# Performance work log

Measured on AMD Instinct MI355X. Metric: run time of the kernel, lower is better.

## Reference

```python
import jax, jax.numpy as jnp
import numpy as np

N, SEQ_LEN, HORIZON, F_IN, EMBED, HIDDEN, LAYERS = 4096, 168, 24, 32, 32, 64, 2
G4 = 4 * HIDDEN
# NOTE: original torch code calls nn.LSTM per-step WITHOUT carrying hidden state,
# so each step's LSTM starts from (h0=0, c0=0): W_hh contributes nothing, only b_hh.

def setup_inputs() -> dict:
    key = jax.random.key(0)
    ks = jax.random.split(key, 12)
    s = 0.1
    return {
        "X": jax.random.normal(ks[0], (N, SEQ_LEN, F_IN), jnp.float32),
        "y": jax.random.normal(ks[1], (N, SEQ_LEN), jnp.float32),
        "Xf": jax.random.normal(ks[2], (N, HORIZON, F_IN), jnp.float32),
        "W_embed": jax.random.normal(ks[3], (EMBED, 1), jnp.float32) * s,
        "b_embed": jax.random.normal(ks[4], (EMBED,), jnp.float32) * s,
        "W_ih": jax.random.normal(ks[5], (LAYERS, G4, EMBED + F_IN), jnp.float32) * s,  # layer1 in-dim == HIDDEN == EMBED+F_IN
        "b_ih": jax.random.normal(ks[6], (LAYERS, G4), jnp.float32) * s,
        "b_hh": jax.random.normal(ks[7], (LAYERS, G4), jnp.float32) * s,
        "W_mu": jax.random.normal(ks[8], (1, HIDDEN), jnp.float32) * s,
        "b_mu": jax.random.normal(ks[9], (1,), jnp.float32) * s,
        "W_sigma": jax.random.normal(ks[10], (1, HIDDEN), jnp.float32) * s,
        "b_sigma": jax.random.normal(ks[11], (1,), jnp.float32) * s,
    }


def reference(X, y, Xf, W_embed, b_embed, W_ih, b_ih, b_hh, W_mu, b_mu, W_sigma, b_sigma):
    num_ts = X.shape[0]
    T = SEQ_LEN + HORIZON
    Xall = jnp.concatenate([X, Xf], axis=1)  # (N, T, F_IN)
    y_pad = jnp.concatenate([y, jnp.zeros((num_ts, HORIZON), y.dtype)], axis=1)  # (N, T)
    use_y = jnp.arange(T) < SEQ_LEN  # teacher-forced region

    def step(carry, inputs):
        x_s, y_s, use = inputs  # (N, F_IN), (N,), scalar bool
        ynext = jnp.where(use, y_s[:, None], carry)  # (N, 1)
        yembed = ynext @ W_embed.T + b_embed  # (N, EMBED)
        h = jnp.concatenate([x_s, yembed], axis=1)  # (N, F_IN+EMBED)
        for l in range(LAYERS):  # single LSTM step from zero state per layer
            gates = h @ W_ih[l].T + b_ih[l] + b_hh[l]  # (N, 4H); torch gate order i,f,g,o
            i_g, f_g, g_g, o_g = jnp.split(gates, 4, axis=1)
            c = jax.nn.sigmoid(i_g) * jnp.tanh(g_g)  # f * c0 term vanishes (c0 = 0)
            h = jax.nn.sigmoid(o_g) * jnp.tanh(c)
        h = jax.nn.relu(h)
        mu = h @ W_mu.T + b_mu  # (N, 1)
        sigma = jax.nn.softplus(h @ W_sigma.T + b_sigma) + 1e-6  # log(1+exp(.)) + eps
        lik = (2.0 * np.pi * sigma ** 2) ** (-0.5) * jnp.exp(-((ynext - mu) ** 2) / (2.0 * sigma ** 2))
        return lik, (lik[:, 0], mu[:, 0], sigma[:, 0])

    carry0 = jnp.zeros((num_ts, 1), X.dtype)
    xs = (jnp.swapaxes(Xall, 0, 1), y_pad.T, use_y)
    _, (lik_t, mu_t, sigma_t) = jax.lax.scan(step, carry0, xs)  # each (T, N)
    ypred = lik_t.T[:, SEQ_LEN - 1: SEQ_LEN + HORIZON - 1]  # (N, HORIZON)
    return ypred, mu_t.T, sigma_t.T
```

## Files before the change

kernel.cpp:

```cpp
#include <hip/hip_runtime.h>
#include <math.h>

#define N_TS 4096
#define SEQ  168
#define HOR  24
#define T_ALL 192
#define F_INP 32
#define HID  64
#define NROW 192
#define HPAD 72

typedef _Float16 half8  __attribute__((ext_vector_type(8)));
typedef _Float16 half4  __attribute__((ext_vector_type(4)));
typedef float    floatx4 __attribute__((ext_vector_type(4)));

__device__ __forceinline__ float fexp(float x)  { return __expf(x); }
__device__ __forceinline__ float frcp(float x)  { return __builtin_amdgcn_rcpf(x); }
__device__ __forceinline__ float softplus_(float x) { return (x > 15.0f) ? x : __logf(1.0f + fexp(x)); }

__device__ __forceinline__ float lstm_h(float ipre, float gpre, float opre) {
    const float Ei = fexp(ipre);
    const float Eg = fexp(gpre);
    const float cc = (1.0f - Eg) * frcp((1.0f + Ei) * (1.0f + Eg));
    const float Ec = fexp(-2.0f * cc);
    const float Eo = fexp(opre);
    return (1.0f - Ec) * frcp((1.0f + Ec) * (1.0f + Eo));
}

__device__ __forceinline__ half8 cvt8(const float4 a, const float4 b) {
    half8 v;
    v[0]=(_Float16)a.x; v[1]=(_Float16)a.y; v[2]=(_Float16)a.z; v[3]=(_Float16)a.w;
    v[4]=(_Float16)b.x; v[5]=(_Float16)b.y; v[6]=(_Float16)b.z; v[7]=(_Float16)b.w;
    return v;
}

__global__ __launch_bounds__(256) void prep(
    const float* __restrict__ W_ih, const float* __restrict__ b_ih,
    const float* __restrict__ b_hh,
    const float* __restrict__ W_embed, const float* __restrict__ b_embed,
    _Float16* __restrict__ W16f, float* __restrict__ bsum,
    float* __restrict__ wy1, float* __restrict__ b1c)
{
    const int idx = blockIdx.x * 256 + threadIdx.x;
    for (int i = idx; i < 2 * 8 * NROW * 8; i += gridDim.x * 256) {
        const int kp  = i & 7;
        const int row = (i >> 3) % NROW;
        const int kb  = ((i >> 3) / NROW) & 7;
        const int l   = i / (8 * NROW * 8);
        const int sr  = (row < 64) ? row : row + 64;
        const float sc = (row >= 64 && row < 128) ? -2.0f : -1.0f;
        W16f[i] = (_Float16)(W_ih[(l * 256 + sr) * HID + kb * 8 + kp] * sc);
    }
    for (int i = idx; i < 2 * NROW; i += gridDim.x * 256) {
        const int r = i % NROW;
        const int l = i / NROW;
        const int sr = (r < 64) ? r : r + 64;
        const float sc = (r >= 64 && r < 128) ? -2.0f : -1.0f;
        bsum[i] = (b_ih[l * 256 + sr] + b_hh[l * 256 + sr]) * sc;
    }
    if (idx < NROW) {
        const int sr = (idx < 64) ? idx : idx + 64;
        const float sc = (idx >= 64 && idx < 128) ? -2.0f : -1.0f;
        const float* wrow = W_ih + sr * HID + 32;
        float s1 = 0.f, s2 = 0.f;
        #pragma unroll
        for (int k = 0; k < 32; ++k) {
            s1 = fmaf(wrow[k], W_embed[k], s1);
            s2 = fmaf(wrow[k], b_embed[k], s2);
        }
        wy1[idx] = s1 * sc;
        b1c[idx] = (b_ih[sr] + b_hh[sr] + s2) * sc;
    }
}

__global__ __launch_bounds__(256, 4) void cellsA(
    const float* __restrict__ X,
    const float* __restrict__ y,
    const float* __restrict__ W_embed,
    const float* __restrict__ b_embed,
    const _Float16* __restrict__ W16f,
    const float* __restrict__ bsum,
    const float* __restrict__ W_mu,
    const float* __restrict__ b_mu,
    const float* __restrict__ W_sigma,
    const float* __restrict__ b_sigma,
    float* __restrict__ out,
    float* __restrict__ lik167)
{
    __shared__ __align__(16) _Float16 Wl[NROW * HID];
    __shared__ __align__(16) _Float16 Hx[4][16 * HPAD];
    const int tid  = threadIdx.x;
    const int w    = tid >> 6;
    const int lane = tid & 63;
    const int quad = lane >> 4;
    const int ln   = lane & 15;
    const int cid0 = blockIdx.x * 64 + w * 16;
    const int cid  = cid0 + ln;

    half8 afr0, afr1;
    {
        const float* xp = X + (size_t)cid * F_INP + quad * 8;
        const float4 xa = *(const float4*)xp;
        const float4 xb = *(const float4*)(xp + 4);
        afr0 = cvt8(xa, xb);
        const float yv = y[cid];
        const float4 wa = *(const float4*)(W_embed + quad * 8);
        const float4 wb = *(const float4*)(W_embed + quad * 8 + 4);
        const float4 ba = *(const float4*)(b_embed + quad * 8);
        const float4 bb = *(const float4*)(b_embed + quad * 8 + 4);
        afr1[0]=(_Float16)fmaf(yv, wa.x, ba.x); afr1[1]=(_Float16)fmaf(yv, wa.y, ba.y);
        afr1[2]=(_Float16)fmaf(yv, wa.z, ba.z); afr1[3]=(_Float16)fmaf(yv, wa.w, ba.w);
        afr1[4]=(_Float16)fmaf(yv, wb.x, bb.x); afr1[5]=(_Float16)fmaf(yv, wb.y, bb.y);
        afr1[6]=(_Float16)fmaf(yv, wb.z, bb.z); afr1[7]=(_Float16)fmaf(yv, wb.w, bb.w);
    }

    #pragma unroll
    for (int c = 0; c < 6; ++c) {
        const int off = (c * 256 + tid) * 8;
        *(half8*)(Wl + off) = *(const half8*)(W16f + off);
    }
    __syncthreads();

    _Float16* hrow = Hx[w];
    {
        floatx4 acc[12];
        #pragma unroll
        for (int nt = 0; nt < 12; ++nt) {
            const float bv = bsum[nt * 16 + ln];
            acc[nt] = (floatx4){bv, bv, bv, bv};
        }
        const _Float16* bp = Wl + quad * 1536 + ln * 8;
        #pragma unroll
        for (int nt = 0; nt < 12; ++nt) {
            const half8 b0 = *(const half8*)(bp + nt * 128);
            const half8 b1 = *(const half8*)(bp + nt * 128 + 6144);
            acc[nt] = __builtin_amdgcn_mfma_f32_16x16x32_f16(afr0, b0, acc[nt], 0, 0, 0);
            acc[nt] = __builtin_amdgcn_mfma_f32_16x16x32_f16(afr1, b1, acc[nt], 0, 0, 0);
        }
        #pragma unroll
        for (int jt = 0; jt < 4; ++jt)
        #pragma unroll
        for (int r = 0; r < 4; ++r) {
            const float hh = lstm_h(acc[jt][r], acc[4 + jt][r], acc[8 + jt][r]);
            hrow[(quad * 4 + r) * HPAD + jt * 16 + ln] = (_Float16)hh;
        }
    }
    __syncthreads();

    #pragma unroll
    for (int c = 0; c < 6; ++c) {
        const int off = (c * 256 + tid) * 8;
        *(half8*)(Wl + off) = *(const half8*)(W16f + 12288 + off);
    }
    __syncthreads();

    float hfin[4][4];
    {
        const half8 a0 = *(const half8*)(hrow + ln * HPAD + quad * 8);
        const half8 a1 = *(const half8*)(hrow + ln * HPAD + 32 + quad * 8);
        floatx4 acc[12];
        #pragma unroll
        for (int nt = 0; nt < 12; ++nt) {
            const float bv = bsum[NROW + nt * 16 + ln];
            acc[nt] = (floatx4){bv, bv, bv, bv};
        }
        const _Float16* bp = Wl + quad * 1536 + ln * 8;
        #pragma unroll
        for (int nt = 0; nt < 12; ++nt) {
            const half8 b0 = *(const half8*)(bp + nt * 128);
            const half8 b1 = *(const half8*)(bp + nt * 128 + 6144);
            acc[nt] = __builtin_amdgcn_mfma_f32_16x16x32_f16(a0, b0, acc[nt], 0, 0, 0);
            acc[nt] = __builtin_amdgcn_mfma_f32_16x16x32_f16(a1, b1, acc[nt], 0, 0, 0);
        }
        #pragma unroll
        for (int jt = 0; jt < 4; ++jt)
        #pragma unroll
        for (int r = 0; r < 4; ++r)
            hfin[jt][r] = lstm_h(acc[jt][r], acc[4 + jt][r], acc[8 + jt][r]);
    }

    float wmu[4], wsg[4];
    #pragma unroll
    for (int jt = 0; jt < 4; ++jt) {
        wmu[jt] = W_mu[jt * 16 + ln];
        wsg[jt] = W_sigma[jt * 16 + ln];
    }
    const float bmu = b_mu[0], bsg = b_sigma[0];
    float* mu_out = out + (size_t)N_TS * HOR;
    float* sg_out = mu_out + (size_t)N_TS * T_ALL;

    #pragma unroll
    for (int r = 0; r < 4; ++r) {
        float pm = 0.f, ps = 0.f;
        #pragma unroll
        for (int jt = 0; jt < 4; ++jt) {
            const float hr = fmaxf(hfin[jt][r], 0.0f);
            pm = fmaf(hr, wmu[jt], pm);
            ps = fmaf(hr, wsg[jt], ps);
        }
        #pragma unroll
        for (int off = 1; off < 16; off <<= 1) {
            pm += __shfl_xor(pm, off, 64);
            ps += __shfl_xor(ps, off, 64);
        }
        if (ln == 0) {
            const int cid2 = cid0 + quad * 4 + r;
            const int n = cid2 / SEQ;
            const int t = cid2 - n * SEQ;
            const float mu = pm + bmu;
            const float sg = softplus_(ps + bsg) + 1e-6f;
            mu_out[(size_t)n * T_ALL + t] = mu;
            sg_out[(size_t)n * T_ALL + t] = sg;
            if (t == SEQ - 1) {
                const float yv = y[cid2];
                const float d  = yv - mu;
                const float is = frcp(sg);
                const float lik = 0.39894228040143267f * is * fexp(-0.5f * d * d * is * is);
                out[(size_t)n * HOR] = lik;
                lik167[n] = lik;
            }
        }
    }
}

__global__ __launch_bounds__(256, 1) void cellsB(
    const float* __restrict__ Xf,
    const _Float16* __restrict__ W16f,
    const float* __restrict__ bsum,
    const float* __restrict__ wy1,
    const float* __restrict__ b1c,
    const float* __restrict__ W_mu,
    const float* __restrict__ b_mu,
    const float* __restrict__ W_sigma,
    const float* __restrict__ b_sigma,
    float* __restrict__ out,
    const float* __restrict__ lik167)
{
    __shared__ __align__(16) _Float16 Hx[16][HPAD];
    __shared__ __align__(16) float partm[16][4];
    __shared__ __align__(16) float parts[16][4];
    __shared__ float ylds[16];

    const int tid  = threadIdx.x;
    const int w    = tid >> 6;
    const int lane = tid & 63;
    const int quad = lane >> 4;
    const int ln   = lane & 15;
    const int n0   = blockIdx.x * 16;

    half8 B1[3];
    half8 B2[3][2];
    #pragma unroll
    for (int j = 0; j < 3; ++j) {
        const int rt = j * 4 + w;
        B1[j] = *(const half8*)(W16f + ((size_t)quad * NROW + rt * 16 + ln) * 8);
        #pragma unroll
        for (int kt = 0; kt < 2; ++kt)
            B2[j][kt] = *(const half8*)(W16f + 12288 + ((size_t)(kt * 4 + quad) * NROW + rt * 16 + ln) * 8);
    }
    float4 wyv[3], b1cv[3];
    #pragma unroll
    for (int g = 0; g < 3; ++g) {
        wyv[g]  = *(const float4*)(wy1 + g * 64 + w * 16 + quad * 4);
        b1cv[g] = *(const float4*)(b1c + g * 64 + w * 16 + quad * 4);
    }
    float bias2[3];
    #pragma unroll
    for (int j = 0; j < 3; ++j)
        bias2[j] = bsum[NROW + (j * 4 + w) * 16 + ln];
    const float wmu = W_mu[w * 16 + ln], wsg = W_sigma[w * 16 + ln];
    const float bmu = b_mu[0], bsg = b_sigma[0];

    if (tid < 16) ylds[tid] = lik167[n0 + tid];
    __syncthreads();

    float* mu_out = out + (size_t)N_TS * HOR;
    float* sg_out = mu_out + (size_t)N_TS * T_ALL;

    const float* xbase = Xf + (size_t)(n0 + ln) * HOR * F_INP + quad * 8;
    float4 xa = *(const float4*)xbase;
    float4 xb = *(const float4*)(xbase + 4);

    #pragma unroll 1
    for (int s = 0; s < HOR; ++s) {
        const half8 xf = cvt8(xa, xb);
        if (s < HOR - 1) {
            xa = *(const float4*)(xbase + (s + 1) * F_INP);
            xb = *(const float4*)(xbase + (s + 1) * F_INP + 4);
        }

        floatx4 t0, t1, t2;
        #pragma unroll
        for (int r = 0; r < 4; ++r) {
            t0[r] = ((const float*)&b1cv[0])[r];
            t1[r] = ((const float*)&b1cv[1])[r];
            t2[r] = ((const float*)&b1cv[2])[r];
        }
        t0 = __builtin_amdgcn_mfma_f32_16x16x32_f16(B1[0], xf, t0, 0, 0, 0);
        t1 = __builtin_amdgcn_mfma_f32_16x16x32_f16(B1[1], xf, t1, 0, 0, 0);
        t2 = __builtin_amdgcn_mfma_f32_16x16x32_f16(B1[2], xf, t2, 0, 0, 0);

        const float yn = ylds[ln];
        half4 h1p;
        #pragma unroll
        for (int r = 0; r < 4; ++r) {
            const float ig = fmaf(yn, ((const float*)&wyv[0])[r], t0[r]);
            const float gg = fmaf(yn, ((const float*)&wyv[1])[r], t1[r]);
            const float og = fmaf(yn, ((const float*)&wyv[2])[r], t2[r]);
            h1p[r] = (_Float16)lstm_h(ig, gg, og);
        }
        *(half4*)(&Hx[ln][w * 16 + quad * 4]) = h1p;
        __syncthreads();

        const half8 a0 = *(const half8*)(&Hx[ln][quad * 8]);
        const half8 a1 = *(const half8*)(&Hx[ln][32 + quad * 8]);
        floatx4 acc[3];
        #pragma unroll
        for (int j = 0; j < 3; ++j) {
            acc[j] = (floatx4){bias2[j], bias2[j], bias2[j], bias2[j]};
            acc[j] = __builtin_amdgcn_mfma_f32_16x16x32_f16(a0, B2[j][0], acc[j], 0, 0, 0);
            acc[j] = __builtin_amdgcn_mfma_f32_16x16x32_f16(a1, B2[j][1], acc[j], 0, 0, 0);
        }

        float pmr[4], psr[4];
        #pragma unroll
        for (int r = 0; r < 4; ++r) {
            const float hh = lstm_h(acc[0][r], acc[1][r], acc[2][r]);
            const float hr = fmaxf(hh, 0.0f);
            pmr[r] = hr * wmu;
            psr[r] = hr * wsg;
        }
        #pragma unroll
        for (int off = 1; off < 16; off <<= 1) {
            #pragma unroll
            for (int r = 0; r < 4; ++r) {
                pmr[r] += __shfl_xor(pmr[r], off, 64);
                psr[r] += __shfl_xor(psr[r], off, 64);
            }
        }
        if (ln == 0) {
            #pragma unroll
            for (int r = 0; r < 4; ++r) {
                partm[quad * 4 + r][w] = pmr[r];
                parts[quad * 4 + r][w] = psr[r];
            }
        }
        __syncthreads();

        if (tid < 16) {
            const float4 m4 = *(const float4*)partm[tid];
            const float4 s4 = *(const float4*)parts[tid];
            const float mu = (m4.x + m4.y) + (m4.z + m4.w) + bmu;
            const float sg = softplus_((s4.x + s4.y) + (s4.z + s4.w) + bsg) + 1e-6f;
            const float yv = ylds[tid];
            const float d  = yv - mu;
            const float is = frcp(sg);
            const float lik = 0.39894228040143267f * is * fexp(-0.5f * d * d * is * is);
            const int nn = n0 + tid;
            const int t  = SEQ + s;
            mu_out[(size_t)nn * T_ALL + t] = mu;
            sg_out[(size_t)nn * T_ALL + t] = sg;
            if (s < HOR - 1) out[(size_t)nn * HOR + s + 1] = lik;
            ylds[tid] = lik;
        }
        __syncthreads();
    }
}

extern "C" void kernel_launch(void* const* d_in, const int* in_sizes, int n_in,
                              void* d_out, int out_size, void* d_ws, size_t ws_size,
                              hipStream_t stream) {
    const float* X       = (const float*)d_in[0];
    const float* y       = (const float*)d_in[1];
    const float* Xf      = (const float*)d_in[2];
    const float* W_embed = (const float*)d_in[3];
    const float* b_embed = (const float*)d_in[4];
    const float* W_ih    = (const float*)d_in[5];
    const float* b_ih    = (const float*)d_in[6];
    const float* b_hh    = (const float*)d_in[7];
    const float* W_mu    = (const float*)d_in[8];
    const float* b_mu    = (const float*)d_in[9];
    const float* W_sigma = (const float*)d_in[10];
    const float* b_sigma = (const float*)d_in[11];

    float* out = (float*)d_out;
    float*     lik167 = (float*)d_ws;
    _Float16*  W16f   = (_Float16*)((char*)d_ws + 16384);
    float*     bsum   = (float*)((char*)d_ws + 16384 + 49152);
    float*     wy1    = (float*)((char*)d_ws + 16384 + 49152 + 1536);
    float*     b1c    = (float*)((char*)d_ws + 16384 + 49152 + 1536 + 768);

    prep<<<96, 256, 0, stream>>>(W_ih, b_ih, b_hh, W_embed, b_embed, W16f, bsum, wy1, b1c);

    cellsA<<<(N_TS * SEQ) / 64, 256, 0, stream>>>(
        X, y, W_embed, b_embed, W16f, bsum,
        W_mu, b_mu, W_sigma, b_sigma, out, lik167);

    cellsB<<<N_TS / 16, 256, 0, stream>>>(
        Xf, W16f, bsum, wy1, b1c,
        W_mu, b_mu, W_sigma, b_sigma, out, lik167);
}
```

Before: 266.9 us.

## Fold log2e into gate weights and run forecast tail as single-wave blocks

Gate weights and biases are pre-scaled by log2(e) in prep, so every LSTM sigmoid/tanh can call the hardware exp2 directly instead of __expf, which saves a multiply per exponential in both cell kernels. The forecast kernel cellsB is rebuilt so one 64-lane wave handles all 192 gate rows for 16 series. Every weight fragment sits in registers, and the per-step __syncthreads and LDS partial-sum reductions are replaced by intra-wave shuffles. The y-embedding is now computed per step and fed as a second MFMA K-slice instead of being folded into precomputed wy1/b1c. The trade-offs are much higher register pressure, twice as many layer-1 MFMAs, and only 256 single-wave blocks on the GPU for the serial 24-step tail.

```diff
diff --git a/kernel.cpp b/kernel.cpp
--- a/kernel.cpp
+++ b/kernel.cpp
@@ -9,21 +9,23 @@
 #define HID  64
 #define NROW 192
 #define HPAD 72
+#define L2E  1.44269504089f
 
 typedef _Float16 half8  __attribute__((ext_vector_type(8)));
 typedef _Float16 half4  __attribute__((ext_vector_type(4)));
 typedef float    floatx4 __attribute__((ext_vector_type(4)));
 
 __device__ __forceinline__ float fexp(float x)  { return __expf(x); }
+__device__ __forceinline__ float ex2(float x)   { return __builtin_amdgcn_exp2f(x); }
 __device__ __forceinline__ float frcp(float x)  { return __builtin_amdgcn_rcpf(x); }
 __device__ __forceinline__ float softplus_(float x) { return (x > 15.0f) ? x : __logf(1.0f + fexp(x)); }
 
-__device__ __forceinline__ float lstm_h(float ipre, float gpre, float opre) {
-    const float Ei = fexp(ipre);
-    const float Eg = fexp(gpre);
+__device__ __forceinline__ float lstm_h(float ip, float gp, float op) {
+    const float Ei = ex2(ip);
+    const float Eg = ex2(gp);
     const float cc = (1.0f - Eg) * frcp((1.0f + Ei) * (1.0f + Eg));
-    const float Ec = fexp(-2.0f * cc);
-    const float Eo = fexp(opre);
+    const float Ec = ex2(cc * (-2.0f * L2E));
+    const float Eo = ex2(op);
     return (1.0f - Ec) * frcp((1.0f + Ec) * (1.0f + Eo));
 }
 
@@ -37,9 +39,7 @@
 __global__ __launch_bounds__(256) void prep(
     const float* __restrict__ W_ih, const float* __restrict__ b_ih,
     const float* __restrict__ b_hh,
-    const float* __restrict__ W_embed, const float* __restrict__ b_embed,
-    _Float16* __restrict__ W16f, float* __restrict__ bsum,
-    float* __restrict__ wy1, float* __restrict__ b1c)
+    _Float16* __restrict__ W16f, float* __restrict__ bsum)
 {
     const int idx = blockIdx.x * 256 + threadIdx.x;
     for (int i = idx; i < 2 * 8 * NROW * 8; i += gridDim.x * 256) {
@@ -48,28 +48,15 @@
         const int kb  = ((i >> 3) / NROW) & 7;
         const int l   = i / (8 * NROW * 8);
         const int sr  = (row < 64) ? row : row + 64;
-        const float sc = (row >= 64 && row < 128) ? -2.0f : -1.0f;
+        const float sc = (row >= 64 && row < 128) ? (-2.0f * L2E) : (-L2E);
         W16f[i] = (_Float16)(W_ih[(l * 256 + sr) * HID + kb * 8 + kp] * sc);
     }
     for (int i = idx; i < 2 * NROW; i += gridDim.x * 256) {
         const int r = i % NROW;
         const int l = i / NROW;
         const int sr = (r < 64) ? r : r + 64;
-        const float sc = (r >= 64 && r < 128) ? -2.0f : -1.0f;
+        const float sc = (r >= 64 && r < 128) ? (-2.0f * L2E) : (-L2E);
         bsum[i] = (b_ih[l * 256 + sr] + b_hh[l * 256 + sr]) * sc;
-    }
-    if (idx < NROW) {
-        const int sr = (idx < 64) ? idx : idx + 64;
-        const float sc = (idx >= 64 && idx < 128) ? -2.0f : -1.0f;
-        const float* wrow = W_ih + sr * HID + 32;
-        float s1 = 0.f, s2 = 0.f;
-        #pragma unroll
-        for (int k = 0; k < 32; ++k) {
-            s1 = fmaf(wrow[k], W_embed[k], s1);
-            s2 = fmaf(wrow[k], b_embed[k], s2);
-        }
-        wy1[idx] = s1 * sc;
-        b1c[idx] = (b_ih[sr] + b_hh[sr] + s2) * sc;
     }
 }
 
@@ -223,12 +210,12 @@
     }
 }
 
-__global__ __launch_bounds__(256, 1) void cellsB(
+__global__ __launch_bounds__(64, 1) void cellsB(
     const float* __restrict__ Xf,
     const _Float16* __restrict__ W16f,
     const float* __restrict__ bsum,
-    const float* __restrict__ wy1,
-    const float* __restrict__ b1c,
+    const float* __restrict__ W_embed,
+    const float* __restrict__ b_embed,
     const float* __restrict__ W_mu,
     const float* __restrict__ b_mu,
     const float* __restrict__ W_sigma,
@@ -236,134 +223,115 @@
     float* __restrict__ out,
     const float* __restrict__ lik167)
 {
-    __shared__ __align__(16) _Float16 Hx[16][HPAD];
-    __shared__ __align__(16) float partm[16][4];
-    __shared__ __align__(16) float parts[16][4];
-    __shared__ float ylds[16];
-
-    const int tid  = threadIdx.x;
-    const int w    = tid >> 6;
-    const int lane = tid & 63;
+    __shared__ __align__(16) _Float16 slab[16][HPAD];
+    const int lane = threadIdx.x;
     const int quad = lane >> 4;
     const int ln   = lane & 15;
     const int n0   = blockIdx.x * 16;
 
-    half8 B1[3];
-    half8 B2[3][2];
-    #pragma unroll
-    for (int j = 0; j < 3; ++j) {
-        const int rt = j * 4 + w;
-        B1[j] = *(const half8*)(W16f + ((size_t)quad * NROW + rt * 16 + ln) * 8);
-        #pragma unroll
-        for (int kt = 0; kt < 2; ++kt)
-            B2[j][kt] = *(const half8*)(W16f + 12288 + ((size_t)(kt * 4 + quad) * NROW + rt * 16 + ln) * 8);
-    }
-    float4 wyv[3], b1cv[3];
-    #pragma unroll
-    for (int g = 0; g < 3; ++g) {
-        wyv[g]  = *(const float4*)(wy1 + g * 64 + w * 16 + quad * 4);
-        b1cv[g] = *(const float4*)(b1c + g * 64 + w * 16 + quad * 4);
-    }
-    float bias2[3];
-    #pragma unroll
-    for (int j = 0; j < 3; ++j)
-        bias2[j] = bsum[NROW + (j * 4 + w) * 16 + ln];
-    const float wmu = W_mu[w * 16 + ln], wsg = W_sigma[w * 16 + ln];
+    half8 W1f[12][2], W2f[12][2];
+    #pragma unroll
+    for (int nt = 0; nt < 12; ++nt)
+        #pragma unroll
+        for (int kf = 0; kf < 2; ++kf) {
+            const int kb = kf * 4 + quad;
+            W1f[nt][kf] = *(const half8*)(W16f + ((size_t)kb * NROW + nt * 16 + ln) * 8);
+            W2f[nt][kf] = *(const half8*)(W16f + 12288 + ((size_t)kb * NROW + nt * 16 + ln) * 8);
+        }
+    float4 b1v[12], b2v[12];
+    #pragma unroll
+    for (int nt = 0; nt < 12; ++nt) {
+        b1v[nt] = *(const float4*)(bsum + nt * 16 + quad * 4);
+        b2v[nt] = *(const float4*)(bsum + NROW + nt * 16 + quad * 4);
+    }
+    float we[8], be[8];
+    #pragma unroll
+    for (int e = 0; e < 8; ++e) {
+        we[e] = W_embed[quad * 8 + e];
+        be[e] = b_embed[quad * 8 + e];
+    }
+    float4 wmuv[4], wsgv[4];
+    #pragma unroll
+    for (int jt = 0; jt < 4; ++jt) {
+        wmuv[jt] = *(const float4*)(W_mu + jt * 16 + quad * 4);
+        wsgv[jt] = *(const float4*)(W_sigma + jt * 16 + quad * 4);
+    }
     const float bmu = b_mu[0], bsg = b_sigma[0];
 
-    if (tid < 16) ylds[tid] = lik167[n0 + tid];
-    __syncthreads();
+    float yv = lik167[n0 + ln];
 
     float* mu_out = out + (size_t)N_TS * HOR;
     float* sg_out = mu_out + (size_t)N_TS * T_ALL;
 
-    const float* xbase = Xf + (size_t)(n0 + ln) * HOR * F_INP + quad * 8;
-    float4 xa = *(const float4*)xbase;
-    float4 xb = *(const float4*)(xbase + 4);
+    const float* xp = Xf + (size_t)(n0 + ln) * HOR * F_INP + quad * 8;
+    float4 xa = *(const float4*)xp;
+    float4 xb = *(const float4*)(xp + 4);
 
     #pragma unroll 1
     for (int s = 0; s < HOR; ++s) {
-        const half8 xf = cvt8(xa, xb);
+        const half8 xf0 = cvt8(xa, xb);
         if (s < HOR - 1) {
-            xa = *(const float4*)(xbase + (s + 1) * F_INP);
-            xb = *(const float4*)(xbase + (s + 1) * F_INP + 4);
-        }
-
-        floatx4 t0, t1, t2;
+            xa = *(const float4*)(xp + (s + 1) * F_INP);
+            xb = *(const float4*)(xp + (s + 1) * F_INP + 4);
+        }
+        half8 xf1;
+        #pragma unroll
+        for (int e = 0; e < 8; ++e)
+            xf1[e] = (_Float16)fmaf(yv, we[e], be[e]);
+
+        floatx4 acc[12];
+        #pragma unroll
+        for (int nt = 0; nt < 12; ++nt) {
+            acc[nt] = (floatx4){b1v[nt].x, b1v[nt].y, b1v[nt].z, b1v[nt].w};
+            acc[nt] = __builtin_amdgcn_mfma_f32_16x16x32_f16(W1f[nt][0], xf0, acc[nt], 0, 0, 0);
+            acc[nt] = __builtin_amdgcn_mfma_f32_16x16x32_f16(W1f[nt][1], xf1, acc[nt], 0, 0, 0);
+        }
+
+        #pragma unroll
+        for (int jt = 0; jt < 4; ++jt) {
+            half4 hp;
+            #pragma unroll
+            for (int r = 0; r < 4; ++r)
+                hp[r] = (_Float16)lstm_h(acc[jt][r], acc[4 + jt][r], acc[8 + jt][r]);
+            *(half4*)(&slab[ln][jt * 16 + quad * 4]) = hp;
+        }
+        const half8 a0 = *(const half8*)(&slab[ln][quad * 8]);
+        const half8 a1 = *(const half8*)(&slab[ln][32 + quad * 8]);
+
+        #pragma unroll
+        for (int nt = 0; nt < 12; ++nt) {
+            acc[nt] = (floatx4){b2v[nt].x, b2v[nt].y, b2v[nt].z, b2v[nt].w};
+            acc[nt] = __builtin_amdgcn_mfma_f32_16x16x32_f16(W2f[nt][0], a0, acc[nt], 0, 0, 0);
+            acc[nt] = __builtin_amdgcn_mfma_f32_16x16x32_f16(W2f[nt][1], a1, acc[nt], 0, 0, 0);
+        }
+
+        float pm = 0.f, ps = 0.f;
+        #pragma unroll
+        for (int jt = 0; jt < 4; ++jt)
         #pragma unroll
         for (int r = 0; r < 4; ++r) {
-            t0[r] = ((const float*)&b1cv[0])[r];
-            t1[r] = ((const float*)&b1cv[1])[r];
-            t2[r] = ((const float*)&b1cv[2])[r];
-        }
-        t0 = __builtin_amdgcn_mfma_f32_16x16x32_f16(B1[0], xf, t0, 0, 0, 0);
-        t1 = __builtin_amdgcn_mfma_f32_16x16x32_f16(B1[1], xf, t1, 0, 0, 0);
-        t2 = __builtin_amdgcn_mfma_f32_16x16x32_f16(B1[2], xf, t2, 0, 0, 0);
-
-        const float yn = ylds[ln];
-        half4 h1p;
-        #pragma unroll
-        for (int r = 0; r < 4; ++r) {
-            const float ig = fmaf(yn, ((const float*)&wyv[0])[r], t0[r]);
-            const float gg = fmaf(yn, ((const float*)&wyv[1])[r], t1[r]);
-            const float og = fmaf(yn, ((const float*)&wyv[2])[r], t2[r]);
-            h1p[r] = (_Float16)lstm_h(ig, gg, og);
-        }
-        *(half4*)(&Hx[ln][w * 16 + quad * 4]) = h1p;
-        __syncthreads();
-
-        const half8 a0 = *(const half8*)(&Hx[ln][quad * 8]);
-        const half8 a1 = *(const half8*)(&Hx[ln][32 + quad * 8]);
-        floatx4 acc[3];
-        #pragma unroll
-        for (int j = 0; j < 3; ++j) {
-            acc[j] = (floatx4){bias2[j], bias2[j], bias2[j], bias2[j]};
-            acc[j] = __builtin_amdgcn_mfma_f32_16x16x32_f16(a0, B2[j][0], acc[j], 0, 0, 0);
-            acc[j] = __builtin_amdgcn_mfma_f32_16x16x32_f16(a1, B2[j][1], acc[j], 0, 0, 0);
-        }
-
-        float pmr[4], psr[4];
-        #pragma unroll
-        for (int r = 0; r < 4; ++r) {
-            const float hh = lstm_h(acc[0][r], acc[1][r], acc[2][r]);
+            const float hh = lstm_h(acc[jt][r], acc[4 + jt][r], acc[8 + jt][r]);
             const float hr = fmaxf(hh, 0.0f);
-            pmr[r] = hr * wmu;
-            psr[r] = hr * wsg;
-        }
-        #pragma unroll
-        for (int off = 1; off < 16; off <<= 1) {
-            #pragma unroll
-            for (int r = 0; r < 4; ++r) {
-                pmr[r] += __shfl_xor(pmr[r], off, 64);
-                psr[r] += __shfl_xor(psr[r], off, 64);
-            }
-        }
-        if (ln == 0) {
-            #pragma unroll
-            for (int r = 0; r < 4; ++r) {
-                partm[quad * 4 + r][w] = pmr[r];
-                parts[quad * 4 + r][w] = psr[r];
-            }
-        }
-        __syncthreads();
-
-        if (tid < 16) {
-            const float4 m4 = *(const float4*)partm[tid];
-            const float4 s4 = *(const float4*)parts[tid];
-            const float mu = (m4.x + m4.y) + (m4.z + m4.w) + bmu;
-            const float sg = softplus_((s4.x + s4.y) + (s4.z + s4.w) + bsg) + 1e-6f;
-            const float yv = ylds[tid];
-            const float d  = yv - mu;
-            const float is = frcp(sg);
-            const float lik = 0.39894228040143267f * is * fexp(-0.5f * d * d * is * is);
-            const int nn = n0 + tid;
+            pm = fmaf(hr, ((const float*)&wmuv[jt])[r], pm);
+            ps = fmaf(hr, ((const float*)&wsgv[jt])[r], ps);
+        }
+        pm += __shfl_xor(pm, 16, 64);  pm += __shfl_xor(pm, 32, 64);
+        ps += __shfl_xor(ps, 16, 64);  ps += __shfl_xor(ps, 32, 64);
+
+        const float mu = pm + bmu;
+        const float sg = softplus_(ps + bsg) + 1e-6f;
+        const float d  = yv - mu;
+        const float is = frcp(sg);
+        const float lik = 0.39894228040143267f * is * fexp(-0.5f * d * d * is * is);
+
+        if (quad == 0) {
+            const int nn = n0 + ln;
             const int t  = SEQ + s;
             mu_out[(size_t)nn * T_ALL + t] = mu;
             sg_out[(size_t)nn * T_ALL + t] = sg;
             if (s < HOR - 1) out[(size_t)nn * HOR + s + 1] = lik;
-            ylds[tid] = lik;
-        }
-        __syncthreads();
+        }
+        yv = lik;
     }
 }
 
@@ -387,16 +355,14 @@
     float*     lik167 = (float*)d_ws;
     _Float16*  W16f   = (_Float16*)((char*)d_ws + 16384);
     float*     bsum   = (float*)((char*)d_ws + 16384 + 49152);
-    float*     wy1    = (float*)((char*)d_ws + 16384 + 49152 + 1536);
-    float*     b1c    = (float*)((char*)d_ws + 16384 + 49152 + 1536 + 768);
-
-    prep<<<96, 256, 0, stream>>>(W_ih, b_ih, b_hh, W_embed, b_embed, W16f, bsum, wy1, b1c);
+
+    prep<<<96, 256, 0, stream>>>(W_ih, b_ih, b_hh, W16f, bsum);
 
     cellsA<<<(N_TS * SEQ) / 64, 256, 0, stream>>>(
         X, y, W_embed, b_embed, W16f, bsum,
         W_mu, b_mu, W_sigma, b_sigma, out, lik167);
 
-    cellsB<<<N_TS / 16, 256, 0, stream>>>(
-        Xf, W16f, bsum, wy1, b1c,
+    cellsB<<<N_TS / 16, 64, 0, stream>>>(
+        Xf, W16f, bsum, W_embed, b_embed,
         W_mu, b_mu, W_sigma, b_sigma, out, lik167);
 }
```

Result: slower. 284.4 us (+6.5%).
